# Optimization experiments

Measured on AMD Instinct MI355X. Metric: run time of the kernel, lower is better.

## Reference

```python
import jax, jax.numpy as jnp
import numpy as np

# Static config matching init_kwargs
WZ, WH, WW = 2, 6, 12          # window size
MZ, MH, MW = 4, 16, 15          # ceil(input_shape / window_size) for (8,96,180)
HEADS, DIM, B = 6, 192, 1
DH = DIM // HEADS
P = WZ * WH * WW                # 144 tokens per window
WN = MZ * MH * MW               # 960 windows
WT = MZ * MH                    # 64 window types
SCALE = DH ** -0.5
TABLE = WZ * WZ * WH * WH * (2 * WW - 1)  # 3312 bias entries


def _position_index():
    zi = np.arange(WZ); zj = -np.arange(WZ) * WZ
    hi = np.arange(WH); hj = -np.arange(WH) * WH
    w = np.arange(WW)
    c1 = np.stack(np.meshgrid(zi, hi, w, indexing='ij')).reshape(3, -1)  # (3, P)
    c2 = np.stack(np.meshgrid(zj, hj, w, indexing='ij')).reshape(3, -1)  # (3, P)
    coords = (c1[:, :, None] - c2[:, None, :]).transpose(1, 2, 0)        # (P, P, 3)
    coords[:, :, 2] += WW - 1
    coords[:, :, 1] *= 2 * WW - 1
    coords[:, :, 0] *= (2 * WW - 1) * WH * WH
    return coords.sum(-1).reshape(-1)  # (P*P,)

POS_IDX = jnp.asarray(_position_index())


def setup_inputs() -> dict:
    key = jax.random.key(0)
    ks = jax.random.split(key, 5)
    x = jax.random.normal(ks[0], (B * WN, P, DIM), dtype=jnp.float32)
    mask = jnp.zeros((WN, P, P), dtype=jnp.float32)
    w_qkv = jax.random.normal(ks[1], (DIM, 3 * DIM), dtype=jnp.float32) * 0.02
    w_proj = jax.random.normal(ks[2], (DIM, DIM), dtype=jnp.float32) * 0.02
    b_proj = jnp.zeros((DIM,), dtype=jnp.float32)
    bias_table = jax.random.normal(ks[3], (TABLE, WT, HEADS), dtype=jnp.float32) * 0.02
    return {"x": x, "mask": mask, "w_qkv": w_qkv, "w_proj": w_proj,
            "b_proj": b_proj, "bias_table": bias_table}


def reference(x, mask, w_qkv, w_proj, b_proj, bias_table):
    BN = x.shape[0]  # B*WN
    qkv = (x @ w_qkv).reshape(BN, P, 3, HEADS, DH).transpose(2, 0, 3, 1, 4)  # (3,BN,h,P,dh)
    q, k, v = SCALE * qkv[0], qkv[1], qkv[2]
    attn = jnp.einsum('bhid,bhjd->bhij', q, k)  # (BN, h, P, P)
    # (B mZ mH mW) h P P -> (B mW) (mZ mH) h P P
    attn = attn.reshape(B, MZ, MH, MW, HEADS, P, P)
    attn = attn.transpose(0, 3, 1, 2, 4, 5, 6).reshape(B * MW, WT, HEADS, P, P)
    # gather earth-specific bias: (P*P, WT, h) -> (WT, h, P, P)
    bias = bias_table[POS_IDX].reshape(P, P, WT, HEADS).transpose(2, 3, 0, 1)
    attn = attn + bias  # broadcast over (B mW)
    # back to (B mZ mH mW) h P P
    attn = attn.reshape(B, MW, MZ, MH, HEADS, P, P)
    attn = attn.transpose(0, 2, 3, 1, 4, 5, 6).reshape(B, WN, HEADS, P, P)
    attn = attn + mask[None, :, None]  # (1, wN, 1, P, P)
    attn = jax.nn.softmax(attn, axis=-1).reshape(B * WN, HEADS, P, P)
    out = jnp.einsum('bhij,bhjd->bhid', attn, v)           # (BN, h, P, dh)
    out = out.transpose(0, 2, 1, 3).reshape(BN, P, DIM)    # merge heads
    return out @ w_proj + b_proj
```

## Files before the change

### kernel.cpp

```cpp
#include <hip/hip_runtime.h>

#define HEADS 6
#define DIM 192
#define DH 32
#define PW 144
#define WN 960
#define MWD 15
#define NTOK (WN*PW)
#define SCALE 0.17677669529663687f
#define LOG2E 1.4426950408889634f
#define SCALE2 (SCALE * LOG2E)

typedef __attribute__((ext_vector_type(8))) short bf16x8;
typedef __attribute__((ext_vector_type(4))) short bf16x4;
typedef __attribute__((ext_vector_type(4))) float f32x4;

#define MFMA16(a,b,c) __builtin_amdgcn_mfma_f32_16x16x32_bf16(a,b,c,0,0,0)

__device__ __forceinline__ unsigned short f2bf(float f) {
    unsigned int u = __builtin_bit_cast(unsigned int, f);
    u += 0x7fffu + ((u >> 16) & 1u);
    return (unsigned short)(u >> 16);
}
__device__ __forceinline__ float bf2f(unsigned short s) {
    unsigned int u = ((unsigned int)s) << 16;
    return __builtin_bit_cast(float, u);
}

__global__ void prep_weights(const float* __restrict__ wqkv,
                             const float* __restrict__ wproj,
                             unsigned short* __restrict__ wqkvT,
                             unsigned short* __restrict__ wprojT) {
    int t = blockIdx.x * 256 + threadIdx.x;
    if (t < 576 * 192) {
        int n = t / 192, k = t % 192;
        wqkvT[t] = f2bf(wqkv[k * 576 + n]);
    } else {
        int t2 = t - 576 * 192;
        int n = t2 / 192, k = t2 % 192;
        wprojT[t2] = f2bf(wproj[k * 192 + n]);
    }
}

__global__ void prep_bias(const float* __restrict__ table,
                          unsigned short* __restrict__ bias_d) {
    int t = blockIdx.x * 256 + threadIdx.x;
    int j = t % 144;
    int i = (t / 144) % 144;
    int h = (t / 20736) % 6;
    int wt = t / 124416;
    int z1 = i / 72, h1 = (i / 12) % 6, w1 = i % 12;
    int z2 = j / 72, h2 = (j / 12) % 6, w2 = j % 12;
    int pos = (z1 + 2 * z2) * 828 + (h1 + 6 * h2) * 23 + (w1 - w2 + 11);
    bias_d[t] = f2bf(table[pos * 384 + wt * 6 + h] * LOG2E);
}

__global__ __launch_bounds__(256) void prep_cast(const float* __restrict__ x,
                                                 unsigned short* __restrict__ xb) {
    long long c = (long long)blockIdx.x * 256 + threadIdx.x;
    const float* p = x + c * 8;
    f32x4 v0 = *(const f32x4*)p;
    f32x4 v1 = *(const f32x4*)(p + 4);
    bf16x8 o;
    o[0] = (short)f2bf(v0[0]); o[1] = (short)f2bf(v0[1]);
    o[2] = (short)f2bf(v0[2]); o[3] = (short)f2bf(v0[3]);
    o[4] = (short)f2bf(v1[0]); o[5] = (short)f2bf(v1[1]);
    o[6] = (short)f2bf(v1[2]); o[7] = (short)f2bf(v1[3]);
    *(bf16x8*)(xb + c * 8) = o;
}

__global__ __launch_bounds__(256) void prep_maskflag(const float* __restrict__ mask,
                                                     int* __restrict__ flags) {
    __shared__ int any;
    if (threadIdx.x == 0) any = 0;
    __syncthreads();
    const float* mp = mask + blockIdx.x * 20736;
    int nz = 0;
    for (int c = threadIdx.x; c < 5184; c += 256) {
        f32x4 v = *(const f32x4*)(mp + c * 4);
        if (v[0] != 0.f || v[1] != 0.f || v[2] != 0.f || v[3] != 0.f) nz = 1;
    }
    if (nz) atomicOr(&any, 1);
    __syncthreads();
    if (threadIdx.x == 0) flags[blockIdx.x] = any;
}

__global__ __launch_bounds__(256) void qkv_gemm(
        const unsigned short* __restrict__ xb, const unsigned short* __restrict__ wqkvT,
        unsigned short* __restrict__ qb, unsigned short* __restrict__ kb,
        unsigned short* __restrict__ vtb) {
    __shared__ unsigned short Bt[96 * 200];
    int bid = blockIdx.x;
    int r8 = bid & 7, s = bid >> 3;
    int nblk = s % 6;
    int mg = r8 * 45 + s / 6;
    int tid = threadIdx.x;
    int lane = tid & 63, wv = tid >> 6;
    int l16 = lane & 15, quad = lane >> 4;

    const unsigned short* wp = wqkvT + nblk * (96 * 192);
    #pragma unroll
    for (int it = 0; it < 9; ++it) {
        int c = tid + it * 256;
        int row = c / 24, c8 = (c % 24) * 8;
        *(bf16x8*)&Bt[row * 200 + c8] = *(const bf16x8*)(wp + c * 8);
    }
    __syncthreads();

    const unsigned short* Abase = xb + ((long long)mg * 6 * 64 + wv * 16 + l16) * 192
                                  + quad * 8;
    bf16x8 a0[6], a1[6];
    #pragma unroll
    for (int kc = 0; kc < 6; ++kc) a0[kc] = *(const bf16x8*)(Abase + kc * 32);

    #pragma unroll
    for (int t = 0; t < 6; ++t) {
        bf16x8* ac = (t & 1) ? a1 : a0;
        bf16x8* an = (t & 1) ? a0 : a1;
        if (t < 5) {
            const unsigned short* Anext = Abase + (long long)(t + 1) * (64 * 192);
            #pragma unroll
            for (int kc = 0; kc < 6; ++kc) an[kc] = *(const bf16x8*)(Anext + kc * 32);
        }
        f32x4 acc[6];
        #pragma unroll
        for (int i = 0; i < 6; ++i) acc[i] = (f32x4){0.f, 0.f, 0.f, 0.f};
        #pragma unroll
        for (int kc = 0; kc < 6; ++kc) {
            bf16x8 af = ac[kc];
            #pragma unroll
            for (int ct = 0; ct < 6; ++ct) {
                bf16x8 bfr = *(const bf16x8*)&Bt[(ct * 16 + l16) * 200 + kc * 32 + quad * 8];
                acc[ct] = MFMA16(af, bfr, acc[ct]);
            }
        }
        int mtile = mg * 6 + t;
        int token0 = mtile * 64 + wv * 16 + quad * 4;
        int win = token0 / 144;
        int p0 = token0 - win * 144;
        #pragma unroll
        for (int ct = 0; ct < 6; ++ct) {
            int c0 = nblk * 96 + ct * 16;
            int which = c0 / 192;
            int head = (c0 % 192) / 32;
            int d = (c0 % 32) + l16;
            if (which == 0) {
                int base = ((win * 6 + head) * 144 + p0) * 32 + d;
                #pragma unroll
                for (int r = 0; r < 4; ++r) qb[base + r * 32] = f2bf(acc[ct][r]);
            } else if (which == 1) {
                int base = ((win * 6 + head) * 144 + p0) * 32 + d;
                #pragma unroll
                for (int r = 0; r < 4; ++r) kb[base + r * 32] = f2bf(acc[ct][r]);
            } else {
                int base = ((win * 6 + head) * 32 + d) * 144 + p0;
                bf16x4 o;
                #pragma unroll
                for (int r = 0; r < 4; ++r) o[r] = (short)f2bf(acc[ct][r]);
                *(bf16x4*)&vtb[base] = o;
            }
        }
    }
}

__global__ __launch_bounds__(192, 3) void attn(
        const unsigned short* __restrict__ qb, const unsigned short* __restrict__ kb,
        const unsigned short* __restrict__ vtb, const unsigned short* __restrict__ bias_d,
        const float* __restrict__ mask, const int* __restrict__ mflags,
        unsigned short* __restrict__ Ob) {
    __shared__ unsigned short Kl[144 * 40];
    __shared__ unsigned short Vt[32 * 168];
    __shared__ unsigned short Pl[3 * 16 * 168];

    int bx = blockIdx.x;
    int r8 = bx & 7, s = bx >> 3;
    int h = s % 6;
    int win = r8 * 120 + s / 6;
    int wt = win / MWD;
    int tid = threadIdx.x;
    int lane = tid & 63, wv = tid >> 6;
    int l16 = lane & 15, quad = lane >> 4;

    int qoff = (win * 6 + h) * (144 * 32);
    #pragma unroll
    for (int it = 0; it < 3; ++it) {
        int c = tid + it * 192;
        int row = c >> 2, c8 = (c & 3) * 8;
        *(bf16x8*)&Kl[row * 40 + c8] = *(const bf16x8*)(kb + qoff + c * 8);
        int vr = c / 18, vc = (c % 18) * 8;
        *(bf16x8*)&Vt[vr * 168 + vc] = *(const bf16x8*)(vtb + qoff + c * 8);
    }
    bf16x8 qreg[3];
    #pragma unroll
    for (int rt = 0; rt < 3; ++rt)
        qreg[rt] = *(const bf16x8*)(qb + qoff + (((wv * 3 + rt) * 16) + l16) * 32 + quad * 8);
    {
        int row = lane >> 2, ch = lane & 3;
        *(bf16x4*)&Pl[wv * 2688 + row * 168 + 144 + ch * 4] = (bf16x4){0, 0, 0, 0};
    }
    if (tid < 96) {
        int row = tid / 3, off = 144 + (tid % 3) * 8;
        *(bf16x8*)&Vt[row * 168 + off] = (bf16x8){0, 0, 0, 0, 0, 0, 0, 0};
    }
    int mflag = mflags[win];
    __syncthreads();

    const float* maskp = mask + win * 20736;
    const unsigned short* biasp = bias_d + (wt * 6 + h) * 20736;
    const f32x4 z = {0.f, 0.f, 0.f, 0.f};
    int pb = wv * 2688;

    #pragma unroll
    for (int rt = 0; rt < 3; ++rt) {
        int i0 = (wv * 3 + rt) * 16;
        int ibase = (i0 + quad * 4) * 144 + l16;
        f32x4 bm[9];
        if (mflag) {
            #pragma unroll
            for (int ct = 0; ct < 9; ++ct) {
                #pragma unroll
                for (int r = 0; r < 4; ++r) {
                    int off = ibase + r * 144 + ct * 16;
                    bm[ct][r] = fmaf(maskp[off], LOG2E, bf2f(biasp[off]));
                }
            }
        } else {
            #pragma unroll
            for (int ct = 0; ct < 9; ++ct) {
                #pragma unroll
                for (int r = 0; r < 4; ++r) {
                    int off = ibase + r * 144 + ct * 16;
                    bm[ct][r] = bf2f(biasp[off]);
                }
            }
        }
        bf16x8 aq = qreg[rt];
        f32x4 sreg[9];
        #pragma unroll
        for (int ct = 0; ct < 9; ++ct) {
            bf16x8 bk = *(const bf16x8*)&Kl[(ct * 16 + l16) * 40 + quad * 8];
            sreg[ct] = MFMA16(aq, bk, z);
        }
        #pragma unroll
        for (int ct = 0; ct < 9; ++ct) {
            #pragma unroll
            for (int r = 0; r < 4; ++r)
                sreg[ct][r] = fmaf(sreg[ct][r], SCALE2, bm[ct][r]);
        }
        float inv[4];
        #pragma unroll
        for (int r = 0; r < 4; ++r) {
            float mx = sreg[0][r];
            #pragma unroll
            for (int ct = 1; ct < 9; ++ct) mx = fmaxf(mx, sreg[ct][r]);
            #pragma unroll
            for (int off = 1; off < 16; off <<= 1) mx = fmaxf(mx, __shfl_xor(mx, off, 64));
            float sum = 0.f;
            #pragma unroll
            for (int ct = 0; ct < 9; ++ct) {
                float e = __builtin_amdgcn_exp2f(sreg[ct][r] - mx);
                sreg[ct][r] = e; sum += e;
            }
            #pragma unroll
            for (int off = 1; off < 16; off <<= 1) sum += __shfl_xor(sum, off, 64);
            inv[r] = __builtin_amdgcn_rcpf(sum);
        }
        #pragma unroll
        for (int ct = 0; ct < 9; ++ct) {
            #pragma unroll
            for (int r = 0; r < 4; ++r)
                Pl[pb + (quad * 4 + r) * 168 + ct * 16 + l16] = f2bf(sreg[ct][r]);
        }
        f32x4 o0 = z, o1 = z;
        #pragma unroll
        for (int kc = 0; kc < 5; ++kc) {
            bf16x8 ap = *(const bf16x8*)&Pl[pb + l16 * 168 + kc * 32 + quad * 8];
            bf16x8 b0 = *(const bf16x8*)&Vt[l16 * 168 + kc * 32 + quad * 8];
            bf16x8 b1 = *(const bf16x8*)&Vt[(16 + l16) * 168 + kc * 32 + quad * 8];
            o0 = MFMA16(ap, b0, o0);
            o1 = MFMA16(ap, b1, o1);
        }
        #pragma unroll
        for (int r = 0; r < 4; ++r) {
            int i = i0 + quad * 4 + r;
            int ob = (win * 144 + i) * 192 + h * 32 + l16;
            Ob[ob] = f2bf(o0[r] * inv[r]);
            Ob[ob + 16] = f2bf(o1[r] * inv[r]);
        }
    }
}

__global__ __launch_bounds__(256) void out_gemm(
        const unsigned short* __restrict__ Ob, const unsigned short* __restrict__ wprojT,
        const float* __restrict__ bproj, float* __restrict__ out) {
    __shared__ unsigned short Bt[96 * 200];
    int bid = blockIdx.x;
    int r8 = bid & 7, s = bid >> 3;
    int nblk = s % 2;
    int mg = r8 * 45 + s / 2;
    int tid = threadIdx.x;
    int lane = tid & 63, wv = tid >> 6;
    int l16 = lane & 15, quad = lane >> 4;

    const unsigned short* wp = wprojT + nblk * (96 * 192);
    #pragma unroll
    for (int it = 0; it < 9; ++it) {
        int c = tid + it * 256;
        int row = c / 24, c8 = (c % 24) * 8;
        *(bf16x8*)&Bt[row * 200 + c8] = *(const bf16x8*)(wp + c * 8);
    }
    __syncthreads();

    const unsigned short* Abase = Ob + ((long long)mg * 6 * 64 + wv * 16 + l16) * 192
                                  + quad * 8;
    bf16x8 a0[6], a1[6];
    #pragma unroll
    for (int kc = 0; kc < 6; ++kc) a0[kc] = *(const bf16x8*)(Abase + kc * 32);

    #pragma unroll
    for (int t = 0; t < 6; ++t) {
        bf16x8* ac = (t & 1) ? a1 : a0;
        bf16x8* an = (t & 1) ? a0 : a1;
        if (t < 5) {
            const unsigned short* Anext = Abase + (long long)(t + 1) * (64 * 192);
            #pragma unroll
            for (int kc = 0; kc < 6; ++kc) an[kc] = *(const bf16x8*)(Anext + kc * 32);
        }
        f32x4 acc[6];
        #pragma unroll
        for (int i = 0; i < 6; ++i) acc[i] = (f32x4){0.f, 0.f, 0.f, 0.f};
        #pragma unroll
        for (int kc = 0; kc < 6; ++kc) {
            bf16x8 af = ac[kc];
            #pragma unroll
            for (int ct = 0; ct < 6; ++ct) {
                bf16x8 bfr = *(const bf16x8*)&Bt[(ct * 16 + l16) * 200 + kc * 32 + quad * 8];
                acc[ct] = MFMA16(af, bfr, acc[ct]);
            }
        }
        int token0 = (mg * 6 + t) * 64 + wv * 16 + quad * 4;
        #pragma unroll
        for (int ct = 0; ct < 6; ++ct) {
            int c = nblk * 96 + ct * 16 + l16;
            float bp = bproj[c];
            #pragma unroll
            for (int r = 0; r < 4; ++r)
                out[(token0 + r) * 192 + c] = acc[ct][r] + bp;
        }
    }
}

extern "C" void kernel_launch(void* const* d_in, const int* in_sizes, int n_in,
                              void* d_out, int out_size, void* d_ws, size_t ws_size,
                              hipStream_t stream) {
    const float* x     = (const float*)d_in[0];
    const float* mask  = (const float*)d_in[1];
    const float* wqkv  = (const float*)d_in[2];
    const float* wproj = (const float*)d_in[3];
    const float* bproj = (const float*)d_in[4];
    const float* btab  = (const float*)d_in[5];
    float* out = (float*)d_out;
    int* mflags = (int*)d_out;

    char* ws = (char*)d_ws;
    unsigned short* xb     = (unsigned short*)(ws + 0);
    unsigned short* Ob     = (unsigned short*)(ws + 0);
    unsigned short* qb     = (unsigned short*)(ws + 53084160);
    unsigned short* kb     = (unsigned short*)(ws + 106168320);
    unsigned short* vtb    = (unsigned short*)(ws + 159252480);
    unsigned short* bias_d = (unsigned short*)(ws + 212336640);
    unsigned short* wqkvT  = (unsigned short*)(ws + 228261888);
    unsigned short* wprojT = (unsigned short*)(ws + 228483072);

    prep_weights<<<576, 256, 0, stream>>>(wqkv, wproj, wqkvT, wprojT);
    prep_bias<<<31104, 256, 0, stream>>>(btab, bias_d);
    prep_maskflag<<<960, 256, 0, stream>>>(mask, mflags);
    prep_cast<<<12960, 256, 0, stream>>>(x, xb);
    qkv_gemm<<<2160, 256, 0, stream>>>(xb, wqkvT, qb, kb, vtb);
    attn<<<5760, 192, 0, stream>>>(qb, kb, vtb, bias_d, mask, mflags, Ob);
    out_gemm<<<720, 256, 0, stream>>>(Ob, wprojT, bproj, out);
}
```

Measured before the change: 450.3 us.

## Fuse QKV projection into attention kernel and merge prep kernels

The four preprocessing kernels are merged into one launch. The QKV GEMM is fused into the attention kernel: each block handles one window, loops over its 6 heads, and computes Q/K/V for each head directly into shared memory. This removes the global round trip of q, k and v, about 160MB of bf16 traffic. In exchange the grid drops from 5760 to 960 blocks of 192 threads, the weight fragments are reloaded from global memory per head, and the heads are serialized with barriers, which may reduce parallelism and latency hiding.

```diff
diff --git a/kernel.cpp b/kernel.cpp
--- a/kernel.cpp
+++ b/kernel.cpp
@@ -27,173 +27,91 @@
     return __builtin_bit_cast(float, u);
 }
 
-__global__ void prep_weights(const float* __restrict__ wqkv,
-                             const float* __restrict__ wproj,
-                             unsigned short* __restrict__ wqkvT,
-                             unsigned short* __restrict__ wprojT) {
-    int t = blockIdx.x * 256 + threadIdx.x;
-    if (t < 576 * 192) {
-        int n = t / 192, k = t % 192;
-        wqkvT[t] = f2bf(wqkv[k * 576 + n]);
+__global__ __launch_bounds__(256) void prep_all(
+        const float* __restrict__ x, const float* __restrict__ mask,
+        const float* __restrict__ wqkv, const float* __restrict__ wproj,
+        const float* __restrict__ btab,
+        unsigned short* __restrict__ xb, unsigned short* __restrict__ bias_d,
+        unsigned short* __restrict__ wqkvT, unsigned short* __restrict__ wprojT,
+        int* __restrict__ flags) {
+    __shared__ int any;
+    int b = blockIdx.x;
+    if (b < 12960) {
+        long long c = (long long)b * 256 + threadIdx.x;
+        const float* p = x + c * 8;
+        f32x4 v0 = *(const f32x4*)p;
+        f32x4 v1 = *(const f32x4*)(p + 4);
+        bf16x8 o;
+        o[0] = (short)f2bf(v0[0]); o[1] = (short)f2bf(v0[1]);
+        o[2] = (short)f2bf(v0[2]); o[3] = (short)f2bf(v0[3]);
+        o[4] = (short)f2bf(v1[0]); o[5] = (short)f2bf(v1[1]);
+        o[6] = (short)f2bf(v1[2]); o[7] = (short)f2bf(v1[3]);
+        *(bf16x8*)(xb + c * 8) = o;
+    } else if (b < 44064) {
+        int t = (b - 12960) * 256 + threadIdx.x;
+        int j = t % 144;
+        int i = (t / 144) % 144;
+        int h = (t / 20736) % 6;
+        int wt = t / 124416;
+        int z1 = i / 72, h1 = (i / 12) % 6, w1 = i % 12;
+        int z2 = j / 72, h2 = (j / 12) % 6, w2 = j % 12;
+        int pos = (z1 + 2 * z2) * 828 + (h1 + 6 * h2) * 23 + (w1 - w2 + 11);
+        bias_d[t] = f2bf(btab[pos * 384 + wt * 6 + h] * LOG2E);
+    } else if (b < 45024) {
+        int w = b - 44064;
+        if (threadIdx.x == 0) any = 0;
+        __syncthreads();
+        const float* mp = mask + w * 20736;
+        int nz = 0;
+        for (int c = threadIdx.x; c < 5184; c += 256) {
+            f32x4 v = *(const f32x4*)(mp + c * 4);
+            if (v[0] != 0.f || v[1] != 0.f || v[2] != 0.f || v[3] != 0.f) nz = 1;
+        }
+        if (nz) atomicOr(&any, 1);
+        __syncthreads();
+        if (threadIdx.x == 0) flags[w] = any;
     } else {
-        int t2 = t - 576 * 192;
-        int n = t2 / 192, k = t2 % 192;
-        wprojT[t2] = f2bf(wproj[k * 192 + n]);
-    }
-}
-
-__global__ void prep_bias(const float* __restrict__ table,
-                          unsigned short* __restrict__ bias_d) {
-    int t = blockIdx.x * 256 + threadIdx.x;
-    int j = t % 144;
-    int i = (t / 144) % 144;
-    int h = (t / 20736) % 6;
-    int wt = t / 124416;
-    int z1 = i / 72, h1 = (i / 12) % 6, w1 = i % 12;
-    int z2 = j / 72, h2 = (j / 12) % 6, w2 = j % 12;
-    int pos = (z1 + 2 * z2) * 828 + (h1 + 6 * h2) * 23 + (w1 - w2 + 11);
-    bias_d[t] = f2bf(table[pos * 384 + wt * 6 + h] * LOG2E);
-}
-
-__global__ __launch_bounds__(256) void prep_cast(const float* __restrict__ x,
-                                                 unsigned short* __restrict__ xb) {
-    long long c = (long long)blockIdx.x * 256 + threadIdx.x;
-    const float* p = x + c * 8;
-    f32x4 v0 = *(const f32x4*)p;
-    f32x4 v1 = *(const f32x4*)(p + 4);
-    bf16x8 o;
-    o[0] = (short)f2bf(v0[0]); o[1] = (short)f2bf(v0[1]);
-    o[2] = (short)f2bf(v0[2]); o[3] = (short)f2bf(v0[3]);
-    o[4] = (short)f2bf(v1[0]); o[5] = (short)f2bf(v1[1]);
-    o[6] = (short)f2bf(v1[2]); o[7] = (short)f2bf(v1[3]);
-    *(bf16x8*)(xb + c * 8) = o;
-}
-
-__global__ __launch_bounds__(256) void prep_maskflag(const float* __restrict__ mask,
-                                                     int* __restrict__ flags) {
-    __shared__ int any;
-    if (threadIdx.x == 0) any = 0;
-    __syncthreads();
-    const float* mp = mask + blockIdx.x * 20736;
-    int nz = 0;
-    for (int c = threadIdx.x; c < 5184; c += 256) {
-        f32x4 v = *(const f32x4*)(mp + c * 4);
-        if (v[0] != 0.f || v[1] != 0.f || v[2] != 0.f || v[3] != 0.f) nz = 1;
-    }
-    if (nz) atomicOr(&any, 1);
-    __syncthreads();
-    if (threadIdx.x == 0) flags[blockIdx.x] = any;
-}
-
-__global__ __launch_bounds__(256) void qkv_gemm(
+        int t = (b - 45024) * 256 + threadIdx.x;
+        if (t < 576 * 192) {
+            int n = t / 192, k = t % 192;
+            wqkvT[t] = f2bf(wqkv[k * 576 + n]);
+        } else {
+            int t2 = t - 576 * 192;
+            int n = t2 / 192, k = t2 % 192;
+            wprojT[t2] = f2bf(wproj[k * 192 + n]);
+        }
+    }
+}
+
+#define STORE_QK(DST, A, M) { \
+    int tok_ = wv * 48 + (M) * 16 + quad * 4; \
+    DST[(tok_ + 0) * 40 + col] = f2bf((A)[0]); \
+    DST[(tok_ + 1) * 40 + col] = f2bf((A)[1]); \
+    DST[(tok_ + 2) * 40 + col] = f2bf((A)[2]); \
+    DST[(tok_ + 3) * 40 + col] = f2bf((A)[3]); }
+#define STORE_V(A, M) { \
+    int tok_ = wv * 48 + (M) * 16 + quad * 4; \
+    bf16x4 o_; \
+    o_[0] = (short)f2bf((A)[0]); o_[1] = (short)f2bf((A)[1]); \
+    o_[2] = (short)f2bf((A)[2]); o_[3] = (short)f2bf((A)[3]); \
+    *(bf16x4*)&Vt[col * 168 + tok_] = o_; }
+
+__global__ __launch_bounds__(192, 3) void qkv_attn(
         const unsigned short* __restrict__ xb, const unsigned short* __restrict__ wqkvT,
-        unsigned short* __restrict__ qb, unsigned short* __restrict__ kb,
-        unsigned short* __restrict__ vtb) {
-    __shared__ unsigned short Bt[96 * 200];
-    int bid = blockIdx.x;
-    int r8 = bid & 7, s = bid >> 3;
-    int nblk = s % 6;
-    int mg = r8 * 45 + s / 6;
-    int tid = threadIdx.x;
-    int lane = tid & 63, wv = tid >> 6;
-    int l16 = lane & 15, quad = lane >> 4;
-
-    const unsigned short* wp = wqkvT + nblk * (96 * 192);
-    #pragma unroll
-    for (int it = 0; it < 9; ++it) {
-        int c = tid + it * 256;
-        int row = c / 24, c8 = (c % 24) * 8;
-        *(bf16x8*)&Bt[row * 200 + c8] = *(const bf16x8*)(wp + c * 8);
-    }
-    __syncthreads();
-
-    const unsigned short* Abase = xb + ((long long)mg * 6 * 64 + wv * 16 + l16) * 192
-                                  + quad * 8;
-    bf16x8 a0[6], a1[6];
-    #pragma unroll
-    for (int kc = 0; kc < 6; ++kc) a0[kc] = *(const bf16x8*)(Abase + kc * 32);
-
-    #pragma unroll
-    for (int t = 0; t < 6; ++t) {
-        bf16x8* ac = (t & 1) ? a1 : a0;
-        bf16x8* an = (t & 1) ? a0 : a1;
-        if (t < 5) {
-            const unsigned short* Anext = Abase + (long long)(t + 1) * (64 * 192);
-            #pragma unroll
-            for (int kc = 0; kc < 6; ++kc) an[kc] = *(const bf16x8*)(Anext + kc * 32);
-        }
-        f32x4 acc[6];
-        #pragma unroll
-        for (int i = 0; i < 6; ++i) acc[i] = (f32x4){0.f, 0.f, 0.f, 0.f};
-        #pragma unroll
-        for (int kc = 0; kc < 6; ++kc) {
-            bf16x8 af = ac[kc];
-            #pragma unroll
-            for (int ct = 0; ct < 6; ++ct) {
-                bf16x8 bfr = *(const bf16x8*)&Bt[(ct * 16 + l16) * 200 + kc * 32 + quad * 8];
-                acc[ct] = MFMA16(af, bfr, acc[ct]);
-            }
-        }
-        int mtile = mg * 6 + t;
-        int token0 = mtile * 64 + wv * 16 + quad * 4;
-        int win = token0 / 144;
-        int p0 = token0 - win * 144;
-        #pragma unroll
-        for (int ct = 0; ct < 6; ++ct) {
-            int c0 = nblk * 96 + ct * 16;
-            int which = c0 / 192;
-            int head = (c0 % 192) / 32;
-            int d = (c0 % 32) + l16;
-            if (which == 0) {
-                int base = ((win * 6 + head) * 144 + p0) * 32 + d;
-                #pragma unroll
-                for (int r = 0; r < 4; ++r) qb[base + r * 32] = f2bf(acc[ct][r]);
-            } else if (which == 1) {
-                int base = ((win * 6 + head) * 144 + p0) * 32 + d;
-                #pragma unroll
-                for (int r = 0; r < 4; ++r) kb[base + r * 32] = f2bf(acc[ct][r]);
-            } else {
-                int base = ((win * 6 + head) * 32 + d) * 144 + p0;
-                bf16x4 o;
-                #pragma unroll
-                for (int r = 0; r < 4; ++r) o[r] = (short)f2bf(acc[ct][r]);
-                *(bf16x4*)&vtb[base] = o;
-            }
-        }
-    }
-}
-
-__global__ __launch_bounds__(192, 3) void attn(
-        const unsigned short* __restrict__ qb, const unsigned short* __restrict__ kb,
-        const unsigned short* __restrict__ vtb, const unsigned short* __restrict__ bias_d,
-        const float* __restrict__ mask, const int* __restrict__ mflags,
-        unsigned short* __restrict__ Ob) {
+        const unsigned short* __restrict__ bias_d, const float* __restrict__ mask,
+        const int* __restrict__ mflags, unsigned short* __restrict__ Ob) {
+    __shared__ unsigned short Ql[144 * 40];
     __shared__ unsigned short Kl[144 * 40];
     __shared__ unsigned short Vt[32 * 168];
     __shared__ unsigned short Pl[3 * 16 * 168];
 
     int bx = blockIdx.x;
-    int r8 = bx & 7, s = bx >> 3;
-    int h = s % 6;
-    int win = r8 * 120 + s / 6;
+    int win = (bx & 7) * 120 + (bx >> 3);
     int wt = win / MWD;
     int tid = threadIdx.x;
     int lane = tid & 63, wv = tid >> 6;
     int l16 = lane & 15, quad = lane >> 4;
 
-    int qoff = (win * 6 + h) * (144 * 32);
-    #pragma unroll
-    for (int it = 0; it < 3; ++it) {
-        int c = tid + it * 192;
-        int row = c >> 2, c8 = (c & 3) * 8;
-        *(bf16x8*)&Kl[row * 40 + c8] = *(const bf16x8*)(kb + qoff + c * 8);
-        int vr = c / 18, vc = (c % 18) * 8;
-        *(bf16x8*)&Vt[vr * 168 + vc] = *(const bf16x8*)(vtb + qoff + c * 8);
-    }
-    bf16x8 qreg[3];
-    #pragma unroll
-    for (int rt = 0; rt < 3; ++rt)
-        qreg[rt] = *(const bf16x8*)(qb + qoff + (((wv * 3 + rt) * 16) + l16) * 32 + quad * 8);
     {
         int row = lane >> 2, ch = lane & 3;
         *(bf16x4*)&Pl[wv * 2688 + row * 168 + 144 + ch * 4] = (bf16x4){0, 0, 0, 0};
@@ -203,90 +121,129 @@
         *(bf16x8*)&Vt[row * 168 + off] = (bf16x8){0, 0, 0, 0, 0, 0, 0, 0};
     }
     int mflag = mflags[win];
-    __syncthreads();
-
     const float* maskp = mask + win * 20736;
-    const unsigned short* biasp = bias_d + (wt * 6 + h) * 20736;
     const f32x4 z = {0.f, 0.f, 0.f, 0.f};
     int pb = wv * 2688;
 
-    #pragma unroll
-    for (int rt = 0; rt < 3; ++rt) {
-        int i0 = (wv * 3 + rt) * 16;
-        int ibase = (i0 + quad * 4) * 144 + l16;
-        f32x4 bm[9];
-        if (mflag) {
+    const unsigned short* xp = xb + ((long long)win * 144 + wv * 48 + l16) * 192 + quad * 8;
+    const unsigned short* wbase = wqkvT + l16 * 192 + quad * 8;
+
+    for (int h = 0; h < 6; ++h) {
+        const unsigned short* biasp = bias_d + (wt * 6 + h) * 20736;
+        const unsigned short* wh = wbase + h * (32 * 192);
+
+        bf16x8 af[3][6];
+        #pragma unroll
+        for (int m = 0; m < 3; ++m)
+            #pragma unroll
+            for (int kc = 0; kc < 6; ++kc)
+                af[m][kc] = *(const bf16x8*)(xp + m * (16 * 192) + kc * 32);
+
+        bf16x8 bA[6], bB[6];
+        #pragma unroll
+        for (int kc = 0; kc < 6; ++kc) bA[kc] = *(const bf16x8*)(wh + kc * 32);
+
+        #pragma unroll
+        for (int nt = 0; nt < 6; ++nt) {
+            bf16x8* bc = (nt & 1) ? bB : bA;
+            bf16x8* bn = (nt & 1) ? bA : bB;
+            if (nt < 5) {
+                int nrow = ((nt + 1) >> 1) * 192 + ((nt + 1) & 1) * 16;
+                #pragma unroll
+                for (int kc = 0; kc < 6; ++kc)
+                    bn[kc] = *(const bf16x8*)(wh + nrow * 192 + kc * 32);
+            }
+            f32x4 a0 = z, a1 = z, a2 = z;
+            #pragma unroll
+            for (int kc = 0; kc < 6; ++kc) {
+                a0 = MFMA16(af[0][kc], bc[kc], a0);
+                a1 = MFMA16(af[1][kc], bc[kc], a1);
+                a2 = MFMA16(af[2][kc], bc[kc], a2);
+            }
+            int col = (nt & 1) * 16 + l16;
+            if (nt < 2) {
+                STORE_QK(Ql, a0, 0) STORE_QK(Ql, a1, 1) STORE_QK(Ql, a2, 2)
+            } else if (nt < 4) {
+                STORE_QK(Kl, a0, 0) STORE_QK(Kl, a1, 1) STORE_QK(Kl, a2, 2)
+            } else {
+                STORE_V(a0, 0) STORE_V(a1, 1) STORE_V(a2, 2)
+            }
+        }
+        __syncthreads();
+
+        #pragma unroll
+        for (int rt = 0; rt < 3; ++rt) {
+            int i0 = (wv * 3 + rt) * 16;
+            int ibase = (i0 + quad * 4) * 144 + l16;
+            bf16x8 aq = *(const bf16x8*)&Ql[(i0 + l16) * 40 + quad * 8];
+            f32x4 sreg[9];
             #pragma unroll
             for (int ct = 0; ct < 9; ++ct) {
-                #pragma unroll
-                for (int r = 0; r < 4; ++r) {
-                    int off = ibase + r * 144 + ct * 16;
-                    bm[ct][r] = fmaf(maskp[off], LOG2E, bf2f(biasp[off]));
+                bf16x8 bk = *(const bf16x8*)&Kl[(ct * 16 + l16) * 40 + quad * 8];
+                sreg[ct] = MFMA16(aq, bk, z);
+            }
+            if (mflag) {
+                #pragma unroll
+                for (int ct = 0; ct < 9; ++ct) {
+                    #pragma unroll
+                    for (int r = 0; r < 4; ++r) {
+                        int off = ibase + r * 144 + ct * 16;
+                        sreg[ct][r] = fmaf(sreg[ct][r], SCALE2,
+                                           fmaf(maskp[off], LOG2E, bf2f(biasp[off])));
+                    }
                 }
-            }
-        } else {
+            } else {
+                #pragma unroll
+                for (int ct = 0; ct < 9; ++ct) {
+                    #pragma unroll
+                    for (int r = 0; r < 4; ++r) {
+                        int off = ibase + r * 144 + ct * 16;
+                        sreg[ct][r] = fmaf(sreg[ct][r], SCALE2, bf2f(biasp[off]));
+                    }
+                }
+            }
+            float inv[4];
+            #pragma unroll
+            for (int r = 0; r < 4; ++r) {
+                float mx = sreg[0][r];
+                #pragma unroll
+                for (int ct = 1; ct < 9; ++ct) mx = fmaxf(mx, sreg[ct][r]);
+                #pragma unroll
+                for (int off = 1; off < 16; off <<= 1) mx = fmaxf(mx, __shfl_xor(mx, off, 64));
+                float sum = 0.f;
+                #pragma unroll
+                for (int ct = 0; ct < 9; ++ct) {
+                    float e = __builtin_amdgcn_exp2f(sreg[ct][r] - mx);
+                    sreg[ct][r] = e; sum += e;
+                }
+                #pragma unroll
+                for (int off = 1; off < 16; off <<= 1) sum += __shfl_xor(sum, off, 64);
+                inv[r] = __builtin_amdgcn_rcpf(sum);
+            }
             #pragma unroll
             for (int ct = 0; ct < 9; ++ct) {
                 #pragma unroll
-                for (int r = 0; r < 4; ++r) {
-                    int off = ibase + r * 144 + ct * 16;
-                    bm[ct][r] = bf2f(biasp[off]);
-                }
-            }
-        }
-        bf16x8 aq = qreg[rt];
-        f32x4 sreg[9];
-        #pragma unroll
-        for (int ct = 0; ct < 9; ++ct) {
-            bf16x8 bk = *(const bf16x8*)&Kl[(ct * 16 + l16) * 40 + quad * 8];
-            sreg[ct] = MFMA16(aq, bk, z);
-        }
-        #pragma unroll
-        for (int ct = 0; ct < 9; ++ct) {
-            #pragma unroll
-            for (int r = 0; r < 4; ++r)
-                sreg[ct][r] = fmaf(sreg[ct][r], SCALE2, bm[ct][r]);
-        }
-        float inv[4];
-        #pragma unroll
-        for (int r = 0; r < 4; ++r) {
-            float mx = sreg[0][r];
-            #pragma unroll
-            for (int ct = 1; ct < 9; ++ct) mx = fmaxf(mx, sreg[ct][r]);
-            #pragma unroll
-            for (int off = 1; off < 16; off <<= 1) mx = fmaxf(mx, __shfl_xor(mx, off, 64));
-            float sum = 0.f;
-            #pragma unroll
-            for (int ct = 0; ct < 9; ++ct) {
-                float e = __builtin_amdgcn_exp2f(sreg[ct][r] - mx);
-                sreg[ct][r] = e; sum += e;
-            }
-            #pragma unroll
-            for (int off = 1; off < 16; off <<= 1) sum += __shfl_xor(sum, off, 64);
-            inv[r] = __builtin_amdgcn_rcpf(sum);
-        }
-        #pragma unroll
-        for (int ct = 0; ct < 9; ++ct) {
-            #pragma unroll
-            for (int r = 0; r < 4; ++r)
-                Pl[pb + (quad * 4 + r) * 168 + ct * 16 + l16] = f2bf(sreg[ct][r]);
-        }
-        f32x4 o0 = z, o1 = z;
-        #pragma unroll
-        for (int kc = 0; kc < 5; ++kc) {
-            bf16x8 ap = *(const bf16x8*)&Pl[pb + l16 * 168 + kc * 32 + quad * 8];
-            bf16x8 b0 = *(const bf16x8*)&Vt[l16 * 168 + kc * 32 + quad * 8];
-            bf16x8 b1 = *(const bf16x8*)&Vt[(16 + l16) * 168 + kc * 32 + quad * 8];
-            o0 = MFMA16(ap, b0, o0);
-            o1 = MFMA16(ap, b1, o1);
-        }
-        #pragma unroll
-        for (int r = 0; r < 4; ++r) {
-            int i = i0 + quad * 4 + r;
-            int ob = (win * 144 + i) * 192 + h * 32 + l16;
-            Ob[ob] = f2bf(o0[r] * inv[r]);
-            Ob[ob + 16] = f2bf(o1[r] * inv[r]);
-        }
+                for (int r = 0; r < 4; ++r)
+                    Pl[pb + (quad * 4 + r) * 168 + ct * 16 + l16] = f2bf(sreg[ct][r]);
+            }
+            f32x4 o0 = z, o1 = z;
+            #pragma unroll
+            for (int kc = 0; kc < 5; ++kc) {
+                bf16x8 ap = *(const bf16x8*)&Pl[pb + l16 * 168 + kc * 32 + quad * 8];
+                bf16x8 b0 = *(const bf16x8*)&Vt[l16 * 168 + kc * 32 + quad * 8];
+                bf16x8 b1 = *(const bf16x8*)&Vt[(16 + l16) * 168 + kc * 32 + quad * 8];
+                o0 = MFMA16(ap, b0, o0);
+                o1 = MFMA16(ap, b1, o1);
+            }
+            #pragma unroll
+            for (int r = 0; r < 4; ++r) {
+                int i = i0 + quad * 4 + r;
+                int ob = (win * 144 + i) * 192 + h * 32 + l16;
+                Ob[ob] = f2bf(o0[r] * inv[r]);
+                Ob[ob + 16] = f2bf(o1[r] * inv[r]);
+            }
+        }
+        __syncthreads();
     }
 }
 
@@ -364,19 +321,13 @@
 
     char* ws = (char*)d_ws;
     unsigned short* xb     = (unsigned short*)(ws + 0);
-    unsigned short* Ob     = (unsigned short*)(ws + 0);
-    unsigned short* qb     = (unsigned short*)(ws + 53084160);
-    unsigned short* kb     = (unsigned short*)(ws + 106168320);
-    unsigned short* vtb    = (unsigned short*)(ws + 159252480);
-    unsigned short* bias_d = (unsigned short*)(ws + 212336640);
-    unsigned short* wqkvT  = (unsigned short*)(ws + 228261888);
-    unsigned short* wprojT = (unsigned short*)(ws + 228483072);
-
-    prep_weights<<<576, 256, 0, stream>>>(wqkv, wproj, wqkvT, wprojT);
-    prep_bias<<<31104, 256, 0, stream>>>(btab, bias_d);
-    prep_maskflag<<<960, 256, 0, stream>>>(mask, mflags);
-    prep_cast<<<12960, 256, 0, stream>>>(x, xb);
-    qkv_gemm<<<2160, 256, 0, stream>>>(xb, wqkvT, qb, kb, vtb);
-    attn<<<5760, 192, 0, stream>>>(qb, kb, vtb, bias_d, mask, mflags, Ob);
+    unsigned short* Ob     = (unsigned short*)(ws + 53084160);
+    unsigned short* bias_d = (unsigned short*)(ws + 106168320);
+    unsigned short* wqkvT  = (unsigned short*)(ws + 122093568);
+    unsigned short* wprojT = (unsigned short*)(ws + 122314752);
+
+    prep_all<<<45600, 256, 0, stream>>>(x, mask, wqkv, wproj, btab,
+                                        xb, bias_d, wqkvT, wprojT, mflags);
+    qkv_attn<<<960, 192, 0, stream>>>(xb, wqkvT, bias_d, mask, mflags, Ob);
     out_gemm<<<720, 256, 0, stream>>>(Ob, wprojT, bproj, out);
 }
```

New measurement: 520.2 us. 15.5% more time.
